# Kernel tuning notes

Hardware: AMD Instinct MI355X
Metric: run time of the kernel (lower is better)

The kernel has to match this reference:

```python
import jax, jax.numpy as jnp
import numpy as np

N = 100000      # nodes
E = 1600000     # edges
R = 4           # relations
F = 128         # node feature dim
EMB = 128       # embedding size
HID = 256       # hidden size
B = 1024        # number of (nest, food) queries


def setup_inputs() -> dict:
    key = jax.random.key(0)
    ks = jax.random.split(key, 12)
    s1 = 1.0 / np.sqrt(F)
    s2 = 1.0 / np.sqrt(EMB)
    sf = 1.0 / np.sqrt(2 * EMB)
    return {
        "x": jax.random.normal(ks[0], (N, F), jnp.float32),
        "edge_index": jax.random.randint(ks[1], (2, E), 0, N),
        "edge_type": jax.random.randint(ks[2], (E,), 0, R),
        "nest_idx": jax.random.randint(ks[3], (B,), 0, N),
        "food_idx": jax.random.randint(ks[4], (B,), 0, N),
        "W_rel1": jax.random.normal(ks[5], (R, F, EMB), jnp.float32) * s1,
        "W_root1": jax.random.normal(ks[6], (F, EMB), jnp.float32) * s1,
        "b1": jnp.zeros((EMB,), jnp.float32),
        "W_rel2": jax.random.normal(ks[7], (R, EMB, EMB), jnp.float32) * s2,
        "W_root2": jax.random.normal(ks[8], (EMB, EMB), jnp.float32) * s2,
        "b2": jnp.zeros((EMB,), jnp.float32),
        "W_fc": jax.random.normal(ks[9], (2 * EMB, HID), jnp.float32) * sf,
        "b_fc": jnp.zeros((HID,), jnp.float32),
    }


def rgcn_conv(x, src, dst, etype, W_rel, W_root, b):
    # Per-relation transform of all nodes: [N, R, O]
    h = jnp.einsum('nf,rfo->nro', x, W_rel)
    msgs = h[src, etype]                      # [E, O] gather per edge
    # Mean aggregation per (dst, relation), PyG RGCNConv default
    key = dst * R + etype                     # [E]
    deg = jax.ops.segment_sum(jnp.ones((E,), x.dtype), key, num_segments=N * R)
    norm = 1.0 / jnp.maximum(deg, 1.0)
    out = jax.ops.segment_sum(msgs * norm[key][:, None], dst, num_segments=N)
    return out + x @ W_root + b


def reference(x, edge_index, edge_type, nest_idx, food_idx,
              W_rel1, W_root1, b1, W_rel2, W_root2, b2, W_fc, b_fc):
    src, dst = edge_index[0], edge_index[1]
    h = jax.nn.relu(rgcn_conv(x, src, dst, edge_type, W_rel1, W_root1, b1))
    h = rgcn_conv(h, src, dst, edge_type, W_rel2, W_root2, b2)
    combined = jnp.concatenate([h[nest_idx], h[food_idx]], axis=-1)  # [B, 2*EMB]
    return jax.nn.relu(combined @ W_fc + b_fc)                        # [B, HID]
```

## Files before the change

### kernel.cpp

```cpp
#include <hip/hip_runtime.h>
#include <stdint.h>

#define NN 100000
#define NE 1600000
#define NR 4
#define NK (NN * NR)
#define FD 128
#define KA 512
#define KT 640
#define NQ 1024
#define HIDN 256

#define NB 391
#define BSH 8
#define CAPB 8192
#define EPB 4096
#define NBLK1 ((NE + EPB - 1) / EPB)
#define MPAD 100096
#define NCHK (MPAD / 128)

using u16 = unsigned short;
using u32 = unsigned int;
typedef __attribute__((ext_vector_type(8))) __bf16 bf16x8;
typedef __attribute__((ext_vector_type(4))) float f32x4;

__device__ __forceinline__ u16 f2b(float f) {
    u32 u = __builtin_bit_cast(u32, f);
    u32 r = u + 0x7FFFu + ((u >> 16) & 1u);
    return (u16)(r >> 16);
}
__device__ __forceinline__ float b2f_lo(u32 v) { return __builtin_bit_cast(float, v << 16); }
__device__ __forceinline__ float b2f_hi(u32 v) { return __builtin_bit_cast(float, v & 0xFFFF0000u); }
__device__ __forceinline__ u32 pack2(float a, float b) {
    return (u32)f2b(a) | ((u32)f2b(b) << 16);
}
__device__ __forceinline__ void gload_lds16(const void* g, void* l) {
    __builtin_amdgcn_global_load_lds((const __attribute__((address_space(1))) u32*)g,
                                     (__attribute__((address_space(3))) u32*)l, 16, 0, 0);
}

__global__ __launch_bounds__(256) void bucket_scatter(const int* __restrict__ ei,
                                                      const int* __restrict__ et,
                                                      int* __restrict__ bcnt,
                                                      u32* __restrict__ bpack) {
    __shared__ int hist[NB];
    __shared__ int base[NB];
    int t = threadIdx.x;
    for (int i = t; i < NB; i += 256) hist[i] = 0;
    __syncthreads();
    int e0 = blockIdx.x * EPB;
    int rank[16];
    u32 pk[16];
    int bk[16];
#pragma unroll
    for (int j = 0; j < 16; ++j) {
        int e = e0 + j * 256 + t;
        bk[j] = -1;
        if (e < NE) {
            int src = __builtin_nontemporal_load(ei + e);
            int dst = __builtin_nontemporal_load(ei + NE + e);
            int r   = __builtin_nontemporal_load(et + e);
            bk[j] = dst >> BSH;
            pk[j] = (u32)src | ((u32)r << 17) | ((u32)(dst & 255) << 19);
            rank[j] = atomicAdd(&hist[bk[j]], 1);
        }
    }
    __syncthreads();
    for (int i = t; i < NB; i += 256) {
        int h = hist[i];
        base[i] = h ? atomicAdd(&bcnt[i], h) : 0;
    }
    __syncthreads();
#pragma unroll
    for (int j = 0; j < 16; ++j)
        if (bk[j] >= 0) bpack[(size_t)bk[j] * CAPB + base[bk[j]] + rank[j]] = pk[j];
}

__global__ __launch_bounds__(256) void key_scatter(const int* __restrict__ bcnt,
                                                   const u32* __restrict__ bpack,
                                                   int* __restrict__ offs6,
                                                   int* __restrict__ spackY) {
    __shared__ int hist[1024];
    __shared__ int sm[256];
    int b = blockIdx.x, t = threadIdx.x;
    int cnt = bcnt[b];
    const u32* seg = bpack + (size_t)b * CAPB;
#pragma unroll
    for (int j = 0; j < 4; ++j) hist[t + j * 256] = 0;
    __syncthreads();
    for (int i = t; i < cnt; i += 256) atomicAdd(&hist[seg[i] >> 17], 1);
    __syncthreads();
    int t4 = t * 4;
    int h0 = hist[t4], h1 = hist[t4 + 1], h2 = hist[t4 + 2], h3 = hist[t4 + 3];
    int s = h0 + h1 + h2 + h3;
    int sp = (s + 7) & ~7;
    sm[t] = sp;
    __syncthreads();
    for (int o2 = 1; o2 < 256; o2 <<= 1) {
        int n = (t >= o2) ? sm[t - o2] : 0;
        __syncthreads();
        sm[t] += n;
        __syncthreads();
    }
    int bas = b * CAPB + sm[t] - sp;
    int e0 = bas, e1 = e0 + h0, e2 = e1 + h1, e3 = e2 + h2, e4 = e3 + h3, eL = bas + sp;
    int node = (b << 8) + t;
    if (node < NN) {
        int* o = offs6 + (size_t)node * 6;
        o[0] = e0; o[1] = e1; o[2] = e2; o[3] = e3; o[4] = e4; o[5] = eL;
    }
    hist[t4] = e0; hist[t4 + 1] = e1; hist[t4 + 2] = e2; hist[t4 + 3] = e3;
    for (int i = e4; i < eL; ++i) spackY[i] = 5 * NN;
    __syncthreads();
    for (int i = t; i < cnt; i += 256) {
        u32 pk = seg[i];
        int pos = atomicAdd(&hist[pk >> 17], 1);
        spackY[pos] = (int)(pk & 0x1FFFFu) + (int)((pk >> 17) & 3u) * NN;
    }
}

__global__ __launch_bounds__(256) void cvt_bf16(const float* __restrict__ in,
                                                u16* __restrict__ outp, int n) {
    int i = blockIdx.x * 256 + threadIdx.x;
    int idx = i * 4;
    if (idx >= n) return;
    float4 v = *(const float4*)(in + idx);
    u32 lo = (u32)f2b(v.x) | ((u32)f2b(v.y) << 16);
    u32 hi = (u32)f2b(v.z) | ((u32)f2b(v.w) << 16);
    *(uint2*)(outp + idx) = make_uint2(lo, hi);
}

__global__ __launch_bounds__(256) void prep_B5(const float* __restrict__ Wrel,
                                               const float* __restrict__ Wroot,
                                               u16* __restrict__ Bt5) {
    int i = blockIdx.x * 256 + threadIdx.x;
    if (i >= 5 * FD * FD) return;
    int tb = i / (FD * FD);
    int rem = i - tb * (FD * FD);
    int o = rem / FD;
    int k = rem - o * FD;
    float v = (tb < 4) ? Wrel[(size_t)tb * FD * FD + (size_t)k * FD + o]
                       : Wroot[(size_t)k * FD + o];
    Bt5[i] = f2b(v);
}

__global__ __launch_bounds__(256) void prep_B(const float* __restrict__ Wrel,
                                              const float* __restrict__ Wroot,
                                              u16* __restrict__ Bt) {
    int i = blockIdx.x * 256 + threadIdx.x;
    if (i >= FD * KT) return;
    int k = i % KT;
    int o = i / KT;
    float v = (k < 512) ? Wrel[(size_t)k * FD + o] : Wroot[(size_t)(k - 512) * FD + o];
    Bt[i] = f2b(v);
}

__global__ __launch_bounds__(256) void gemm_y(const u16* __restrict__ X,
                                              const u16* __restrict__ Bt5,
                                              u16* __restrict__ Y) {
    __shared__ u16 As[2][8192];
    int blk = blockIdx.x;
    int rel = blk / NCHK;
    int chunk = blk - rel * NCHK;
    int row0 = chunk * 128;
    int tid = threadIdx.x;
    int wid = tid >> 6, lane = tid & 63;
    int wm = wid >> 1, wn = wid & 1;
    int lr = lane & 15, hi = lane >> 4;
    const u16* Btr = Bt5 + (size_t)rel * FD * FD;
    u16* C = Y + (size_t)rel * NN * FD;

    int srow = wid * 8 + (lane >> 3);
    int sg = (lane & 7) ^ ((lane >> 3) & 7);
#pragma unroll
    for (int s = 0; s < 2; ++s)
#pragma unroll
        for (int i = 0; i < 4; ++i) {
            int r = i * 32 + srow;
            int gr = row0 + r;
            gload_lds16(X + (size_t)gr * FD + s * 64 + sg * 8,
                        (char*)As[s] + i * 4096 + wid * 1024);
        }
    __syncthreads();

    f32x4 acc[4][4];
#pragma unroll
    for (int i = 0; i < 4; ++i)
#pragma unroll
        for (int j = 0; j < 4; ++j) acc[i][j] = (f32x4){0.f, 0.f, 0.f, 0.f};

#pragma unroll
    for (int t = 0; t < 2; ++t) {
#pragma unroll
        for (int kk = 0; kk < 2; ++kk) {
            bf16x8 bfr[4], afr[4];
#pragma unroll
            for (int ni = 0; ni < 4; ++ni) {
                int col = wn * 64 + ni * 16 + lr;
                bfr[ni] = *reinterpret_cast<const bf16x8*>(
                    Btr + (size_t)col * FD + t * 64 + kk * 32 + hi * 8);
            }
#pragma unroll
            for (int mi = 0; mi < 4; ++mi) {
                int r = wm * 64 + mi * 16 + lr;
                int sp = (kk * 4 + hi) ^ (r & 7);
                afr[mi] = *reinterpret_cast<const bf16x8*>((char*)As[t] + r * 128 + sp * 16);
            }
#pragma unroll
            for (int mi = 0; mi < 4; ++mi)
#pragma unroll
                for (int ni = 0; ni < 4; ++ni)
                    acc[mi][ni] = __builtin_amdgcn_mfma_f32_16x16x32_bf16(afr[mi], bfr[ni], acc[mi][ni], 0, 0, 0);
        }
    }
#pragma unroll
    for (int mi = 0; mi < 4; ++mi)
#pragma unroll
        for (int ni = 0; ni < 4; ++ni) {
            int col = wn * 64 + ni * 16 + lr;
#pragma unroll
            for (int rg = 0; rg < 4; ++rg) {
                int row = row0 + wm * 64 + mi * 16 + hi * 4 + rg;
                if (row < NN) C[(size_t)row * FD + col] = f2b(acc[mi][ni][rg]);
            }
        }
}

__global__ __launch_bounds__(256) void agg_l1(const int* __restrict__ offs6,
                                              const int* __restrict__ spackY,
                                              const u32* __restrict__ Y,
                                              const float* __restrict__ bias,
                                              u16* __restrict__ h1) {
    int wid = threadIdx.x >> 6, lane = threadIdx.x & 63;
    int node = blockIdx.x * 4 + wid;
    if (node >= NN) return;

    const int* ob = offs6 + (size_t)node * 6;
    int o0 = __builtin_amdgcn_readfirstlane(ob[0]);
    int o1 = __builtin_amdgcn_readfirstlane(ob[1]);
    int o2 = __builtin_amdgcn_readfirstlane(ob[2]);
    int o3 = __builtin_amdgcn_readfirstlane(ob[3]);
    int o4 = __builtin_amdgcn_readfirstlane(ob[4]);
    int oL = __builtin_amdgcn_readfirstlane(ob[5]);

    float a00 = 0, a01 = 0, a10 = 0, a11 = 0, a20 = 0, a21 = 0, a30 = 0, a31 = 0;

    for (int e = o0; e < oL; e += 8) {
        int p[8];
        u32 v[8];
#pragma unroll
        for (int j = 0; j < 8; ++j)
            p[j] = __builtin_amdgcn_readfirstlane(spackY[e + j]);
#pragma unroll
        for (int j = 0; j < 8; ++j) v[j] = Y[(size_t)p[j] * 64 + lane];
#pragma unroll
        for (int j = 0; j < 8; ++j) {
            int ij = e + j;
            float f0 = b2f_lo(v[j]);
            float f1 = b2f_hi(v[j]);
            if (ij < o1)      { a00 += f0; a01 += f1; }
            else if (ij < o2) { a10 += f0; a11 += f1; }
            else if (ij < o3) { a20 += f0; a21 += f1; }
            else              { a30 += f0; a31 += f1; }
        }
    }

    int d0 = o1 - o0, d1 = o2 - o1, d2 = o3 - o2, d3 = o4 - o3;
    float s0 = 1.0f / (float)(d0 > 1 ? d0 : 1);
    float s1 = 1.0f / (float)(d1 > 1 ? d1 : 1);
    float s2 = 1.0f / (float)(d2 > 1 ? d2 : 1);
    float s3 = 1.0f / (float)(d3 > 1 ? d3 : 1);
    float sum0 = a00 * s0 + a10 * s1 + a20 * s2 + a30 * s3;
    float sum1 = a01 * s0 + a11 * s1 + a21 * s2 + a31 * s3;
    u32 rv = Y[((size_t)4 * NN + node) * 64 + lane];
    float2 bb = *reinterpret_cast<const float2*>(bias + lane * 2);
    float r0 = fmaxf(sum0 + b2f_lo(rv) + bb.x, 0.f);
    float r1 = fmaxf(sum1 + b2f_hi(rv) + bb.y, 0.f);
    *(u32*)(h1 + (size_t)node * FD + lane * 2) = pack2(r0, r1);
}

__global__ __launch_bounds__(256) void agg_q(const int* __restrict__ offs6,
                                             const int* __restrict__ spackY,
                                             const u32* __restrict__ fp,
                                             u16* __restrict__ Aout,
                                             const int* __restrict__ nest,
                                             const int* __restrict__ food,
                                             int* __restrict__ qnodes) {
    int wid = threadIdx.x >> 6, lane = threadIdx.x & 63;
    int row = blockIdx.x * 4 + wid;
    if (row >= 2 * NQ) return;
    int node = (row < NQ) ? nest[row] : food[row - NQ];
    node = __builtin_amdgcn_readfirstlane(node);
    if (lane == 0) qnodes[row] = node;
    const int* ob = offs6 + (size_t)node * 6;
    int o[5];
#pragma unroll
    for (int i = 0; i < 5; ++i) o[i] = __builtin_amdgcn_readfirstlane(ob[i]);
    u16* Ao = Aout + (size_t)row * KA + lane * 2;
#pragma unroll
    for (int r = 0; r < 4; ++r) {
        int s = o[r], t = o[r + 1], last = t - 1;
        float a0 = 0, a1 = 0;
        for (int e = s; e < t; e += 8) {
            int p[8];
            u32 v[8];
#pragma unroll
            for (int j = 0; j < 8; ++j) {
                int ij = e + j;
                int cl = ij <= last ? ij : last;
                int pv = __builtin_amdgcn_readfirstlane(spackY[cl]) - r * NN;
                p[j] = (ij <= last) ? pv : NN;
            }
#pragma unroll
            for (int j = 0; j < 8; ++j) v[j] = fp[(size_t)p[j] * 64 + lane];
#pragma unroll
            for (int j = 0; j < 8; ++j) { a0 += b2f_lo(v[j]); a1 += b2f_hi(v[j]); }
        }
        int d = t - s;
        float sc = 1.0f / (float)(d > 1 ? d : 1);
        *(u32*)(Ao + r * 128) = pack2(a0 * sc, a1 * sc);
    }
}

__global__ __launch_bounds__(256) void gemm_lds3(const u16* __restrict__ A,
                                                 const u16* __restrict__ rootSrc,
                                                 const int* __restrict__ rootIdx,
                                                 const u16* __restrict__ Bt,
                                                 const float* __restrict__ bias,
                                                 float* __restrict__ Cout, int M) {
    __shared__ u16 As[3][8192];
    int tid = threadIdx.x;
    int wid = tid >> 6, lane = tid & 63;
    int wm = wid >> 1, wn = wid & 1;
    int lr = lane & 15, hi = lane >> 4;
    int row0 = blockIdx.x * 128;

    f32x4 acc[4][4];
#pragma unroll
    for (int i = 0; i < 4; ++i)
#pragma unroll
        for (int j = 0; j < 4; ++j) acc[i][j] = (f32x4){0.f, 0.f, 0.f, 0.f};

    int srow = wid * 8 + (lane >> 3);
    int sg = (lane & 7) ^ ((lane >> 3) & 7);

    auto stage = [&](int t, int buf) {
#pragma unroll
        for (int i = 0; i < 4; ++i) {
            int r = i * 32 + srow;
            int gr = row0 + r;
            const u16* src;
            if (t < 8) {
                src = A + (size_t)gr * KA + t * 64 + sg * 8;
            } else {
                int idx = rootIdx[gr];
                src = rootSrc + (size_t)idx * FD + (t - 8) * 64 + sg * 8;
            }
            gload_lds16(src, (char*)As[buf] + i * 4096 + wid * 1024);
        }
    };

    stage(0, 0);
    stage(1, 1);

    for (int t = 0; t < 10; ++t) {
        int cur = t % 3;
        bf16x8 bfr[2][4];
#pragma unroll
        for (int kk = 0; kk < 2; ++kk)
#pragma unroll
            for (int ni = 0; ni < 4; ++ni) {
                int col = wn * 64 + ni * 16 + lr;
                bfr[kk][ni] = *reinterpret_cast<const bf16x8*>(
                    Bt + (size_t)col * KT + t * 64 + kk * 32 + hi * 8);
            }
        bool staged = (t + 2 < 10);
        if (staged) stage(t + 2, (t + 2) % 3);
        if (staged) asm volatile("s_waitcnt vmcnt(4)" ::: "memory");
        else        asm volatile("s_waitcnt vmcnt(0)" ::: "memory");
        __builtin_amdgcn_s_barrier();
        __builtin_amdgcn_sched_barrier(0);
#pragma unroll
        for (int kk = 0; kk < 2; ++kk) {
            bf16x8 afr[4];
#pragma unroll
            for (int mi = 0; mi < 4; ++mi) {
                int r = wm * 64 + mi * 16 + lr;
                int sp = (kk * 4 + hi) ^ (r & 7);
                afr[mi] = *reinterpret_cast<const bf16x8*>((char*)As[cur] + r * 128 + sp * 16);
            }
#pragma unroll
            for (int mi = 0; mi < 4; ++mi)
#pragma unroll
                for (int ni = 0; ni < 4; ++ni)
                    acc[mi][ni] = __builtin_amdgcn_mfma_f32_16x16x32_bf16(afr[mi], bfr[kk][ni], acc[mi][ni], 0, 0, 0);
        }
        asm volatile("s_waitcnt lgkmcnt(0)" ::: "memory");
        __builtin_amdgcn_s_barrier();
    }

#pragma unroll
    for (int mi = 0; mi < 4; ++mi)
#pragma unroll
        for (int ni = 0; ni < 4; ++ni) {
            int col = wn * 64 + ni * 16 + lr;
            float bv = bias[col];
#pragma unroll
            for (int rg = 0; rg < 4; ++rg) {
                int row = row0 + wm * 64 + mi * 16 + hi * 4 + rg;
                if (row < M) Cout[(size_t)row * FD + col] = acc[mi][ni][rg] + bv;
            }
        }
}

__global__ __launch_bounds__(256) void fc_kernel(const float* __restrict__ h2q,
                                                 const float* __restrict__ Wfc,
                                                 const float* __restrict__ bfc,
                                                 float* __restrict__ out) {
    __shared__ float comb[2 * FD];
    int q = blockIdx.x, t = threadIdx.x;
    if (t < FD) comb[t] = h2q[(size_t)q * FD + t];
    else comb[t] = h2q[(size_t)(NQ + q) * FD + (t - FD)];
    __syncthreads();
    float s = bfc[t];
#pragma unroll 4
    for (int k = 0; k < 2 * FD; ++k) s += comb[k] * Wfc[(size_t)k * HIDN + t];
    out[(size_t)q * HIDN + t] = fmaxf(s, 0.f);
}

extern "C" void kernel_launch(void* const* d_in, const int* in_sizes, int n_in,
                              void* d_out, int out_size, void* d_ws, size_t ws_size,
                              hipStream_t stream) {
    const float* x      = (const float*)d_in[0];
    const int*   ei     = (const int*)d_in[1];
    const int*   et     = (const int*)d_in[2];
    const int*   nest   = (const int*)d_in[3];
    const int*   food   = (const int*)d_in[4];
    const float* Wrel1  = (const float*)d_in[5];
    const float* Wroot1 = (const float*)d_in[6];
    const float* b1     = (const float*)d_in[7];
    const float* Wrel2  = (const float*)d_in[8];
    const float* Wroot2 = (const float*)d_in[9];
    const float* b2     = (const float*)d_in[10];
    const float* Wfc    = (const float*)d_in[11];
    const float* bfc    = (const float*)d_in[12];
    float* out = (float*)d_out;

    char* w = (char*)d_ws;
    size_t off = 0;
    auto take = [&](size_t b) {
        char* p = w + off;
        off += b;
        off = (off + 255) & ~(size_t)255;
        return p;
    };
    int* bcnt   = (int*)take((size_t)NB * 4);
    int* offs6  = (int*)take((size_t)NN * 6 * 4);
    u32* bpack  = (u32*)take((size_t)NB * CAPB * 4);
    int* spackY = (int*)take((size_t)NB * CAPB * 4);
    int* qnodes = (int*)take((size_t)2 * NQ * 4);
    u16* xh     = (u16*)take((size_t)MPAD * FD * 2);
    u16* h1     = (u16*)take((size_t)MPAD * FD * 2);
    u16* Bt5    = (u16*)take((size_t)5 * FD * FD * 2);
    u16* Bt2    = (u16*)take((size_t)FD * KT * 2);
    u16* Y      = (u16*)take(((size_t)5 * NN + 1) * FD * 2);
    u16* A2     = (u16*)take((size_t)2 * NQ * KA * 2);
    float* h2q  = (float*)take((size_t)2 * NQ * FD * 4);

    hipMemsetAsync(bcnt, 0, (size_t)NB * 4, stream);
    hipMemsetAsync(h1 + (size_t)NN * FD, 0, FD * 2, stream);
    hipMemsetAsync(Y + (size_t)5 * NN * FD, 0, FD * 2, stream);
    cvt_bf16<<<((NN * FD / 4) + 255) / 256, 256, 0, stream>>>(x, xh, NN * FD);
    prep_B5<<<(5 * FD * FD + 255) / 256, 256, 0, stream>>>(Wrel1, Wroot1, Bt5);
    prep_B<<<(FD * KT + 255) / 256, 256, 0, stream>>>(Wrel2, Wroot2, Bt2);

    gemm_y<<<5 * NCHK, 256, 0, stream>>>(xh, Bt5, Y);

    bucket_scatter<<<NBLK1, 256, 0, stream>>>(ei, et, bcnt, bpack);
    key_scatter<<<NB, 256, 0, stream>>>(bcnt, bpack, offs6, spackY);

    agg_l1<<<(NN + 3) / 4, 256, 0, stream>>>(offs6, spackY, (const u32*)Y, b1, h1);

    agg_q<<<(2 * NQ + 3) / 4, 256, 0, stream>>>(offs6, spackY, (const u32*)h1, A2,
                                                nest, food, qnodes);
    gemm_lds3<<<(2 * NQ) / 128, 256, 0, stream>>>(A2, h1, qnodes, Bt2, b2, h2q, 2 * NQ);
    fc_kernel<<<NQ, 256, 0, stream>>>(h2q, Wfc, bfc, out);
}
```

Before: 253.0 us.

## Restrict layer-1 aggregation to the two-hop neighborhood of query nodes

Replaces the full bucket sort of all edges with a pruned pipeline. It marks the query nodes and the sources of edges that point into them, compacts those nodes through bitmap scans, and builds CSR structures only for that subset, with separate layer-1 and layer-2 edge lists. Layer-1 aggregation then runs only on the needed nodes instead of all 100k, and the query-side aggregation gathers from the compacted hidden array. The cost is many extra small kernel launches and three passes over the edge list. It also adds fixed capacities (MAXS, MAXL2) that hold only if the neighborhood stays small enough for these inputs.

```diff
diff --git a/kernel.cpp b/kernel.cpp
--- a/kernel.cpp
+++ b/kernel.cpp
@@ -4,23 +4,23 @@
 #define NN 100000
 #define NE 1600000
 #define NR 4
-#define NK (NN * NR)
 #define FD 128
 #define KA 512
 #define KT 640
 #define NQ 1024
 #define HIDN 256
 
-#define NB 391
-#define BSH 8
-#define CAPB 8192
-#define EPB 4096
-#define NBLK1 ((NE + EPB - 1) / EPB)
 #define MPAD 100096
 #define NCHK (MPAD / 128)
+#define NBE ((NE + 2047) / 2048)
+#define NCHB ((NN + 255) / 256)
+#define MAXS 49152
+#define NCH1 (MAXS / 256)
+#define MAXL2 65536
 
 using u16 = unsigned short;
 using u32 = unsigned int;
+using u8 = unsigned char;
 typedef __attribute__((ext_vector_type(8))) __bf16 bf16x8;
 typedef __attribute__((ext_vector_type(4))) float f32x4;
 
@@ -39,83 +39,257 @@
                                      (__attribute__((address_space(3))) u32*)l, 16, 0, 0);
 }
 
-__global__ __launch_bounds__(256) void bucket_scatter(const int* __restrict__ ei,
-                                                      const int* __restrict__ et,
-                                                      int* __restrict__ bcnt,
-                                                      u32* __restrict__ bpack) {
-    __shared__ int hist[NB];
-    __shared__ int base[NB];
+__global__ __launch_bounds__(256) void mark_T(const int* __restrict__ nest,
+                                              const int* __restrict__ food,
+                                              u8* __restrict__ bmT, u8* __restrict__ bmS) {
+    int i = blockIdx.x * 256 + threadIdx.x;
+    if (i < NQ)          { int q = nest[i];      bmT[q] = 1; bmS[q] = 1; }
+    else if (i < 2 * NQ) { int q = food[i - NQ]; bmT[q] = 1; bmS[q] = 1; }
+}
+
+__global__ __launch_bounds__(256) void filter_l2(const int* __restrict__ ei,
+                                                 const int* __restrict__ et,
+                                                 const u8* __restrict__ bmT,
+                                                 u8* __restrict__ bmS,
+                                                 int* __restrict__ cnts,
+                                                 u32* __restrict__ l2a,
+                                                 u32* __restrict__ l2d) {
+    __shared__ int lcnt, lbase;
+    __shared__ u32 ba[2048], bd[2048];
     int t = threadIdx.x;
-    for (int i = t; i < NB; i += 256) hist[i] = 0;
-    __syncthreads();
-    int e0 = blockIdx.x * EPB;
-    int rank[16];
-    u32 pk[16];
-    int bk[16];
-#pragma unroll
-    for (int j = 0; j < 16; ++j) {
+    if (t == 0) lcnt = 0;
+    __syncthreads();
+    int e0 = blockIdx.x * 2048;
+    for (int j = 0; j < 8; ++j) {
         int e = e0 + j * 256 + t;
-        bk[j] = -1;
         if (e < NE) {
-            int src = __builtin_nontemporal_load(ei + e);
-            int dst = __builtin_nontemporal_load(ei + NE + e);
-            int r   = __builtin_nontemporal_load(et + e);
-            bk[j] = dst >> BSH;
-            pk[j] = (u32)src | ((u32)r << 17) | ((u32)(dst & 255) << 19);
-            rank[j] = atomicAdd(&hist[bk[j]], 1);
-        }
-    }
-    __syncthreads();
-    for (int i = t; i < NB; i += 256) {
-        int h = hist[i];
-        base[i] = h ? atomicAdd(&bcnt[i], h) : 0;
-    }
-    __syncthreads();
-#pragma unroll
-    for (int j = 0; j < 16; ++j)
-        if (bk[j] >= 0) bpack[(size_t)bk[j] * CAPB + base[bk[j]] + rank[j]] = pk[j];
-}
-
-__global__ __launch_bounds__(256) void key_scatter(const int* __restrict__ bcnt,
-                                                   const u32* __restrict__ bpack,
-                                                   int* __restrict__ offs6,
-                                                   int* __restrict__ spackY) {
-    __shared__ int hist[1024];
+            int dst = ei[NE + e];
+            if (bmT[dst]) {
+                int src = ei[e];
+                int r = et[e];
+                int pos = atomicAdd(&lcnt, 1);
+                ba[pos] = (u32)src | ((u32)r << 17);
+                bd[pos] = (u32)dst;
+                bmS[src] = 1;
+            }
+        }
+    }
+    __syncthreads();
+    if (t == 0) lbase = atomicAdd(&cnts[2], lcnt);
+    __syncthreads();
+    for (int i = t; i < lcnt; i += 256) {
+        l2a[lbase + i] = ba[i];
+        l2d[lbase + i] = bd[i];
+    }
+}
+
+__global__ __launch_bounds__(256) void bm_chunk(const u8* __restrict__ bmS,
+                                                const u8* __restrict__ bmT,
+                                                int* __restrict__ cS, int* __restrict__ cT) {
+    __shared__ int sS[256], sT[256];
+    int b = blockIdx.x, t = threadIdx.x;
+    int n = b * 256 + t;
+    int vs = (n < NN) ? bmS[n] : 0;
+    int vt = (n < NN) ? bmT[n] : 0;
+    sS[t] = vs; sT[t] = vt;
+    __syncthreads();
+    for (int o = 128; o > 0; o >>= 1) {
+        if (t < o) { sS[t] += sS[t + o]; sT[t] += sT[t + o]; }
+        __syncthreads();
+    }
+    if (t == 0) { cS[b] = sS[0]; cT[b] = sT[0]; }
+}
+
+__global__ __launch_bounds__(512) void bm_scan(const int* __restrict__ cS,
+                                               const int* __restrict__ cT,
+                                               int* __restrict__ oS, int* __restrict__ oT,
+                                               int* __restrict__ cnts) {
+    __shared__ int sS[512], sT[512];
+    int t = threadIdx.x;
+    int vs = (t < NCHB) ? cS[t] : 0;
+    int vt = (t < NCHB) ? cT[t] : 0;
+    sS[t] = vs; sT[t] = vt;
+    __syncthreads();
+    for (int o = 1; o < 512; o <<= 1) {
+        int a = (t >= o) ? sS[t - o] : 0;
+        int c = (t >= o) ? sT[t - o] : 0;
+        __syncthreads();
+        sS[t] += a; sT[t] += c;
+        __syncthreads();
+    }
+    if (t < NCHB) { oS[t] = sS[t] - vs; oT[t] = sT[t] - vt; }
+    if (t == NCHB - 1) { cnts[0] = sS[t]; cnts[1] = sT[t]; }
+}
+
+__global__ __launch_bounds__(256) void bm_write(const u8* __restrict__ bmS,
+                                                const u8* __restrict__ bmT,
+                                                const int* __restrict__ oS,
+                                                const int* __restrict__ oT,
+                                                int* __restrict__ sid, int* __restrict__ tidm,
+                                                int* __restrict__ snode) {
+    __shared__ int sS[256], sT[256];
+    int b = blockIdx.x, t = threadIdx.x;
+    int n = b * 256 + t;
+    int vs = (n < NN) ? bmS[n] : 0;
+    int vt = (n < NN) ? bmT[n] : 0;
+    sS[t] = vs; sT[t] = vt;
+    __syncthreads();
+    for (int o = 1; o < 256; o <<= 1) {
+        int a = (t >= o) ? sS[t - o] : 0;
+        int c = (t >= o) ? sT[t - o] : 0;
+        __syncthreads();
+        sS[t] += a; sT[t] += c;
+        __syncthreads();
+    }
+    if (n < NN) {
+        int is = oS[b] + sS[t] - vs;
+        int it = oT[b] + sT[t] - vt;
+        sid[n] = is;
+        tidm[n] = it;
+        if (vs) snode[is] = n;
+    }
+}
+
+__global__ __launch_bounds__(256) void l2_count(const int* __restrict__ cnts,
+                                                const u32* __restrict__ l2a,
+                                                const u32* __restrict__ l2d,
+                                                const int* __restrict__ tidm,
+                                                int* __restrict__ deg2) {
+    int n = cnts[2];
+    for (int i = blockIdx.x * 256 + threadIdx.x; i < n; i += gridDim.x * 256)
+        atomicAdd(&deg2[tidm[l2d[i]] * 4 + ((l2a[i] >> 17) & 3)], 1);
+}
+
+__global__ __launch_bounds__(1024) void l2_scan(const int* __restrict__ deg2,
+                                                int* __restrict__ offs2,
+                                                int* __restrict__ cur2) {
+    __shared__ int sm[1024];
+    int t = threadIdx.x;
+    int v[8];
+    int s = 0;
+    for (int j = 0; j < 8; ++j) { v[j] = deg2[t * 8 + j]; s += v[j]; }
+    sm[t] = s;
+    __syncthreads();
+    for (int o = 1; o < 1024; o <<= 1) {
+        int n = (t >= o) ? sm[t - o] : 0;
+        __syncthreads();
+        sm[t] += n;
+        __syncthreads();
+    }
+    int ex = sm[t] - s;
+    for (int j = 0; j < 8; ++j) { offs2[t * 8 + j] = ex; cur2[t * 8 + j] = ex; ex += v[j]; }
+    if (t == 1023) offs2[8192] = ex;
+}
+
+__global__ __launch_bounds__(256) void l2_scatter(const int* __restrict__ cnts,
+                                                  const u32* __restrict__ l2a,
+                                                  const u32* __restrict__ l2d,
+                                                  const int* __restrict__ tidm,
+                                                  const int* __restrict__ sid,
+                                                  int* __restrict__ cur2,
+                                                  int* __restrict__ spack2) {
+    int n = cnts[2];
+    for (int i = blockIdx.x * 256 + threadIdx.x; i < n; i += gridDim.x * 256) {
+        u32 a = l2a[i];
+        int k = tidm[l2d[i]] * 4 + ((a >> 17) & 3);
+        int pos = atomicAdd(&cur2[k], 1);
+        spack2[pos] = sid[a & 0x1FFFFu];
+    }
+}
+
+__global__ __launch_bounds__(256) void l1_count(const int* __restrict__ ei,
+                                                const int* __restrict__ et,
+                                                const u8* __restrict__ bmS,
+                                                const int* __restrict__ sid,
+                                                int* __restrict__ deg1) {
+    int e0 = blockIdx.x * 2048;
+    int t = threadIdx.x;
+    for (int j = 0; j < 8; ++j) {
+        int e = e0 + j * 256 + t;
+        if (e < NE) {
+            int dst = ei[NE + e];
+            if (bmS[dst]) atomicAdd(&deg1[sid[dst] * 4 + et[e]], 1);
+        }
+    }
+}
+
+__global__ __launch_bounds__(256) void l1_chunk(const int* __restrict__ deg1,
+                                                int* __restrict__ c1) {
     __shared__ int sm[256];
     int b = blockIdx.x, t = threadIdx.x;
-    int cnt = bcnt[b];
-    const u32* seg = bpack + (size_t)b * CAPB;
-#pragma unroll
-    for (int j = 0; j < 4; ++j) hist[t + j * 256] = 0;
-    __syncthreads();
-    for (int i = t; i < cnt; i += 256) atomicAdd(&hist[seg[i] >> 17], 1);
-    __syncthreads();
-    int t4 = t * 4;
-    int h0 = hist[t4], h1 = hist[t4 + 1], h2 = hist[t4 + 2], h3 = hist[t4 + 3];
-    int s = h0 + h1 + h2 + h3;
+    int n = b * 256 + t;
+    int s = deg1[4 * n] + deg1[4 * n + 1] + deg1[4 * n + 2] + deg1[4 * n + 3];
+    sm[t] = (s + 7) & ~7;
+    __syncthreads();
+    for (int o = 128; o > 0; o >>= 1) {
+        if (t < o) sm[t] += sm[t + o];
+        __syncthreads();
+    }
+    if (t == 0) c1[b] = sm[0];
+}
+
+__global__ __launch_bounds__(256) void l1_scan(const int* __restrict__ c1,
+                                               int* __restrict__ o1) {
+    __shared__ int sm[256];
+    int t = threadIdx.x;
+    int v = (t < NCH1) ? c1[t] : 0;
+    sm[t] = v;
+    __syncthreads();
+    for (int o = 1; o < 256; o <<= 1) {
+        int n = (t >= o) ? sm[t - o] : 0;
+        __syncthreads();
+        sm[t] += n;
+        __syncthreads();
+    }
+    if (t < NCH1) o1[t] = sm[t] - v;
+}
+
+__global__ __launch_bounds__(256) void l1_write(const int* __restrict__ deg1,
+                                                const int* __restrict__ o1,
+                                                int* __restrict__ offs6s,
+                                                int* __restrict__ cur1,
+                                                int* __restrict__ spack1) {
+    __shared__ int sm[256];
+    int b = blockIdx.x, t = threadIdx.x;
+    int n = b * 256 + t;
+    int d0 = deg1[4 * n], d1 = deg1[4 * n + 1], d2 = deg1[4 * n + 2], d3 = deg1[4 * n + 3];
+    int s = d0 + d1 + d2 + d3;
     int sp = (s + 7) & ~7;
     sm[t] = sp;
     __syncthreads();
-    for (int o2 = 1; o2 < 256; o2 <<= 1) {
-        int n = (t >= o2) ? sm[t - o2] : 0;
-        __syncthreads();
-        sm[t] += n;
-        __syncthreads();
-    }
-    int bas = b * CAPB + sm[t] - sp;
-    int e0 = bas, e1 = e0 + h0, e2 = e1 + h1, e3 = e2 + h2, e4 = e3 + h3, eL = bas + sp;
-    int node = (b << 8) + t;
-    if (node < NN) {
-        int* o = offs6 + (size_t)node * 6;
-        o[0] = e0; o[1] = e1; o[2] = e2; o[3] = e3; o[4] = e4; o[5] = eL;
-    }
-    hist[t4] = e0; hist[t4 + 1] = e1; hist[t4 + 2] = e2; hist[t4 + 3] = e3;
-    for (int i = e4; i < eL; ++i) spackY[i] = 5 * NN;
-    __syncthreads();
-    for (int i = t; i < cnt; i += 256) {
-        u32 pk = seg[i];
-        int pos = atomicAdd(&hist[pk >> 17], 1);
-        spackY[pos] = (int)(pk & 0x1FFFFu) + (int)((pk >> 17) & 3u) * NN;
+    for (int o = 1; o < 256; o <<= 1) {
+        int v = (t >= o) ? sm[t - o] : 0;
+        __syncthreads();
+        sm[t] += v;
+        __syncthreads();
+    }
+    int e0 = o1[b] + sm[t] - sp;
+    int e1 = e0 + d0, e2 = e1 + d1, e3 = e2 + d2, e4 = e3 + d3, eL = e0 + sp;
+    int* o6 = offs6s + (size_t)n * 6;
+    o6[0] = e0; o6[1] = e1; o6[2] = e2; o6[3] = e3; o6[4] = e4; o6[5] = eL;
+    cur1[4 * n] = e0; cur1[4 * n + 1] = e1; cur1[4 * n + 2] = e2; cur1[4 * n + 3] = e3;
+    for (int i = e4; i < eL; ++i) spack1[i] = 5 * NN;
+}
+
+__global__ __launch_bounds__(256) void l1_scatter(const int* __restrict__ ei,
+                                                  const int* __restrict__ et,
+                                                  const u8* __restrict__ bmS,
+                                                  const int* __restrict__ sid,
+                                                  int* __restrict__ cur1,
+                                                  int* __restrict__ spack1) {
+    int e0 = blockIdx.x * 2048;
+    int t = threadIdx.x;
+    for (int j = 0; j < 8; ++j) {
+        int e = e0 + j * 256 + t;
+        if (e < NE) {
+            int dst = ei[NE + e];
+            if (bmS[dst]) {
+                int r = et[e];
+                int src = ei[e];
+                int pos = atomicAdd(&cur1[sid[dst] * 4 + r], 1);
+                spack1[pos] = r * NN + src;
+            }
+        }
     }
 }
 
@@ -226,16 +400,18 @@
         }
 }
 
-__global__ __launch_bounds__(256) void agg_l1(const int* __restrict__ offs6,
-                                              const int* __restrict__ spackY,
-                                              const u32* __restrict__ Y,
-                                              const float* __restrict__ bias,
-                                              u16* __restrict__ h1) {
+__global__ __launch_bounds__(256) void agg_s(const int* __restrict__ cnts,
+                                             const int* __restrict__ offs6s,
+                                             const int* __restrict__ spack1,
+                                             const int* __restrict__ snode,
+                                             const u32* __restrict__ Y,
+                                             const float* __restrict__ bias,
+                                             u16* __restrict__ h1s) {
     int wid = threadIdx.x >> 6, lane = threadIdx.x & 63;
-    int node = blockIdx.x * 4 + wid;
-    if (node >= NN) return;
-
-    const int* ob = offs6 + (size_t)node * 6;
+    int row = blockIdx.x * 4 + wid;
+    if (row >= cnts[0]) return;
+
+    const int* ob = offs6s + (size_t)row * 6;
     int o0 = __builtin_amdgcn_readfirstlane(ob[0]);
     int o1 = __builtin_amdgcn_readfirstlane(ob[1]);
     int o2 = __builtin_amdgcn_readfirstlane(ob[2]);
@@ -250,7 +426,7 @@
         u32 v[8];
 #pragma unroll
         for (int j = 0; j < 8; ++j)
-            p[j] = __builtin_amdgcn_readfirstlane(spackY[e + j]);
+            p[j] = __builtin_amdgcn_readfirstlane(spack1[e + j]);
 #pragma unroll
         for (int j = 0; j < 8; ++j) v[j] = Y[(size_t)p[j] * 64 + lane];
 #pragma unroll
@@ -272,27 +448,31 @@
     float s3 = 1.0f / (float)(d3 > 1 ? d3 : 1);
     float sum0 = a00 * s0 + a10 * s1 + a20 * s2 + a30 * s3;
     float sum1 = a01 * s0 + a11 * s1 + a21 * s2 + a31 * s3;
+    int node = __builtin_amdgcn_readfirstlane(snode[row]);
     u32 rv = Y[((size_t)4 * NN + node) * 64 + lane];
     float2 bb = *reinterpret_cast<const float2*>(bias + lane * 2);
     float r0 = fmaxf(sum0 + b2f_lo(rv) + bb.x, 0.f);
     float r1 = fmaxf(sum1 + b2f_hi(rv) + bb.y, 0.f);
-    *(u32*)(h1 + (size_t)node * FD + lane * 2) = pack2(r0, r1);
-}
-
-__global__ __launch_bounds__(256) void agg_q(const int* __restrict__ offs6,
-                                             const int* __restrict__ spackY,
-                                             const u32* __restrict__ fp,
-                                             u16* __restrict__ Aout,
-                                             const int* __restrict__ nest,
-                                             const int* __restrict__ food,
-                                             int* __restrict__ qnodes) {
+    *(u32*)(h1s + (size_t)row * FD + lane * 2) = pack2(r0, r1);
+}
+
+__global__ __launch_bounds__(256) void agg_q2(const int* __restrict__ offs2,
+                                              const int* __restrict__ spack2,
+                                              const u32* __restrict__ h1s4,
+                                              const int* __restrict__ nest,
+                                              const int* __restrict__ food,
+                                              const int* __restrict__ tidm,
+                                              const int* __restrict__ sid,
+                                              u16* __restrict__ Aout,
+                                              int* __restrict__ sidq) {
     int wid = threadIdx.x >> 6, lane = threadIdx.x & 63;
     int row = blockIdx.x * 4 + wid;
     if (row >= 2 * NQ) return;
-    int node = (row < NQ) ? nest[row] : food[row - NQ];
-    node = __builtin_amdgcn_readfirstlane(node);
-    if (lane == 0) qnodes[row] = node;
-    const int* ob = offs6 + (size_t)node * 6;
+    int q = (row < NQ) ? nest[row] : food[row - NQ];
+    q = __builtin_amdgcn_readfirstlane(q);
+    int tq = __builtin_amdgcn_readfirstlane(tidm[q]);
+    if (lane == 0) sidq[row] = sid[q];
+    const int* ob = offs2 + (size_t)tq * 4;
     int o[5];
 #pragma unroll
     for (int i = 0; i < 5; ++i) o[i] = __builtin_amdgcn_readfirstlane(ob[i]);
@@ -308,11 +488,11 @@
             for (int j = 0; j < 8; ++j) {
                 int ij = e + j;
                 int cl = ij <= last ? ij : last;
-                int pv = __builtin_amdgcn_readfirstlane(spackY[cl]) - r * NN;
-                p[j] = (ij <= last) ? pv : NN;
-            }
-#pragma unroll
-            for (int j = 0; j < 8; ++j) v[j] = fp[(size_t)p[j] * 64 + lane];
+                int pv = __builtin_amdgcn_readfirstlane(spack2[cl]);
+                p[j] = (ij <= last) ? pv : MAXS;
+            }
+#pragma unroll
+            for (int j = 0; j < 8; ++j) v[j] = h1s4[(size_t)p[j] * 64 + lane];
 #pragma unroll
             for (int j = 0; j < 8; ++j) { a0 += b2f_lo(v[j]); a1 += b2f_hi(v[j]); }
         }
@@ -454,35 +634,68 @@
         off = (off + 255) & ~(size_t)255;
         return p;
     };
-    int* bcnt   = (int*)take((size_t)NB * 4);
-    int* offs6  = (int*)take((size_t)NN * 6 * 4);
-    u32* bpack  = (u32*)take((size_t)NB * CAPB * 4);
-    int* spackY = (int*)take((size_t)NB * CAPB * 4);
-    int* qnodes = (int*)take((size_t)2 * NQ * 4);
+    size_t zero0 = off;
+    int* cnts   = (int*)take(256);
+    u8* bmT     = (u8*)take(NN);
+    u8* bmS     = (u8*)take(NN);
+    int* deg2   = (int*)take(8192 * 4);
+    int* deg1   = (int*)take((size_t)4 * MAXS * 4);
+    size_t zeroSz = off - zero0;
+    char* zbase = w + zero0;
+    int* oS     = (int*)take((size_t)NCHB * 4);
+    int* oT     = (int*)take((size_t)NCHB * 4);
+    int* c1     = (int*)take((size_t)NCH1 * 4);
+    int* o1     = (int*)take((size_t)NCH1 * 4);
+    int* sid    = (int*)take((size_t)NN * 4);
+    int* tidm   = (int*)take((size_t)NN * 4);
+    int* snode  = (int*)take((size_t)MAXS * 4);
+    u32* l2a    = (u32*)take((size_t)MAXL2 * 4);
+    u32* l2d    = (u32*)take((size_t)MAXL2 * 4);
+    int* offs2  = (int*)take((size_t)8193 * 4);
+    int* cur2   = (int*)take((size_t)8192 * 4);
+    int* spack2 = (int*)take((size_t)MAXL2 * 4);
+    int* offs6s = (int*)take((size_t)MAXS * 6 * 4);
+    int* cur1   = (int*)take((size_t)4 * MAXS * 4);
+    int* spack1 = (int*)take(((size_t)NE + 8 * MAXS) * 4);
+    int* sidq   = (int*)take((size_t)2 * NQ * 4);
     u16* xh     = (u16*)take((size_t)MPAD * FD * 2);
-    u16* h1     = (u16*)take((size_t)MPAD * FD * 2);
     u16* Bt5    = (u16*)take((size_t)5 * FD * FD * 2);
     u16* Bt2    = (u16*)take((size_t)FD * KT * 2);
     u16* Y      = (u16*)take(((size_t)5 * NN + 1) * FD * 2);
+    u16* h1s    = (u16*)take(((size_t)MAXS + 1) * FD * 2);
     u16* A2     = (u16*)take((size_t)2 * NQ * KA * 2);
     float* h2q  = (float*)take((size_t)2 * NQ * FD * 4);
 
-    hipMemsetAsync(bcnt, 0, (size_t)NB * 4, stream);
-    hipMemsetAsync(h1 + (size_t)NN * FD, 0, FD * 2, stream);
+    hipMemsetAsync(zbase, 0, zeroSz, stream);
     hipMemsetAsync(Y + (size_t)5 * NN * FD, 0, FD * 2, stream);
+    hipMemsetAsync(h1s + (size_t)MAXS * FD, 0, FD * 2, stream);
+
     cvt_bf16<<<((NN * FD / 4) + 255) / 256, 256, 0, stream>>>(x, xh, NN * FD);
     prep_B5<<<(5 * FD * FD + 255) / 256, 256, 0, stream>>>(Wrel1, Wroot1, Bt5);
     prep_B<<<(FD * KT + 255) / 256, 256, 0, stream>>>(Wrel2, Wroot2, Bt2);
 
+    mark_T<<<(2 * NQ + 255) / 256, 256, 0, stream>>>(nest, food, bmT, bmS);
+    filter_l2<<<NBE, 256, 0, stream>>>(ei, et, bmT, bmS, cnts, l2a, l2d);
+    bm_chunk<<<NCHB, 256, 0, stream>>>(bmS, bmT, oS, oT);
+    bm_scan<<<1, 512, 0, stream>>>(oS, oT, oS, oT, cnts);
+    bm_write<<<NCHB, 256, 0, stream>>>(bmS, bmT, oS, oT, sid, tidm, snode);
+
+    l2_count<<<128, 256, 0, stream>>>(cnts, l2a, l2d, tidm, deg2);
+    l2_scan<<<1, 1024, 0, stream>>>(deg2, offs2, cur2);
+    l2_scatter<<<128, 256, 0, stream>>>(cnts, l2a, l2d, tidm, sid, cur2, spack2);
+
+    l1_count<<<NBE, 256, 0, stream>>>(ei, et, bmS, sid, deg1);
+    l1_chunk<<<NCH1, 256, 0, stream>>>(deg1, c1);
+    l1_scan<<<1, 256, 0, stream>>>(c1, o1);
+    l1_write<<<NCH1, 256, 0, stream>>>(deg1, o1, offs6s, cur1, spack1);
+    l1_scatter<<<NBE, 256, 0, stream>>>(ei, et, bmS, sid, cur1, spack1);
+
     gemm_y<<<5 * NCHK, 256, 0, stream>>>(xh, Bt5, Y);
 
-    bucket_scatter<<<NBLK1, 256, 0, stream>>>(ei, et, bcnt, bpack);
-    key_scatter<<<NB, 256, 0, stream>>>(bcnt, bpack, offs6, spackY);
-
-    agg_l1<<<(NN + 3) / 4, 256, 0, stream>>>(offs6, spackY, (const u32*)Y, b1, h1);
-
-    agg_q<<<(2 * NQ + 3) / 4, 256, 0, stream>>>(offs6, spackY, (const u32*)h1, A2,
-                                                nest, food, qnodes);
-    gemm_lds3<<<(2 * NQ) / 128, 256, 0, stream>>>(A2, h1, qnodes, Bt2, b2, h2q, 2 * NQ);
+    agg_s<<<MAXS / 4, 256, 0, stream>>>(cnts, offs6s, spack1, snode, (const u32*)Y, b1, h1s);
+
+    agg_q2<<<(2 * NQ + 3) / 4, 256, 0, stream>>>(offs2, spack2, (const u32*)h1s,
+                                                 nest, food, tidm, sid, A2, sidq);
+    gemm_lds3<<<(2 * NQ) / 128, 256, 0, stream>>>(A2, h1s, sidq, Bt2, b2, h2q, 2 * NQ);
     fc_kernel<<<NQ, 256, 0, stream>>>(h2q, Wfc, bfc, out);
 }
```

Result: slower. 259.3 us (+2.5%).
